# Performance work log

Hardware: AMD Instinct MI355X
Metric: run time of the kernel (lower is better)

Reference implementation:

```python
import jax, jax.numpy as jnp
import numpy as np

N_HEADS = 16

def setup_inputs() -> dict:
    key = jax.random.key(0)
    qkv = jax.random.normal(key, (4, 3072, 1024), dtype=jnp.float32)
    return {"qkv": qkv}

def reference(qkv):
    bs, width, length = qkv.shape
    ch = width // (3 * N_HEADS)
    qkv_h = qkv.reshape(bs * N_HEADS, 3 * ch, length)
    q, k, v = jnp.split(qkv_h, 3, axis=1)  # each [bs*H, ch, T]
    scale = 1.0 / jnp.sqrt(jnp.sqrt(jnp.asarray(ch, qkv.dtype)))
    # [bs*H, T, T] scores
    weight = jnp.einsum('bct,bcs->bts', q * scale, k * scale)
    weight = jax.nn.softmax(weight.astype(jnp.float32), axis=-1).astype(weight.dtype)
    a = jnp.einsum('bts,bcs->bct', weight, v)  # [bs*H, ch, T]
    return a.reshape(bs, -1, length)
```

## Files before the change

### kernel.cpp

```cpp
#include <hip/hip_runtime.h>
#include <hip/hip_bf16.h>


typedef __bf16 bf16_8 __attribute__((ext_vector_type(8)));
typedef __bf16 bf16_4 __attribute__((ext_vector_type(4)));
typedef float floatx4 __attribute__((ext_vector_type(4)));

#define NTHREADS 256
#define STRIDE 72
#define NSTEPS 16

#if __has_builtin(__builtin_amdgcn_exp2f)
#define EXP2(x) __builtin_amdgcn_exp2f(x)
#else
#define EXP2(x) exp2f(x)
#endif
#define QSCALE 0.18033688011112042f

#define LDS_BYTES 36864

__global__ __launch_bounds__(NTHREADS, 2)
void attn_kernel(const float* __restrict__ qkv, float* __restrict__ out) {
    __shared__ char smem[LDS_BYTES];
    __bf16* q_s = (__bf16*)smem;
    __bf16* k_s = (__bf16*)(smem + 18432);
    __bf16* v_s = (__bf16*)(smem + 27648);

    const int tid  = threadIdx.x;
    const int wave = tid >> 6;
    const int lane = tid & 63;
    const int quad = lane >> 4;
    const int i16  = lane & 15;

    const int bx = blockIdx.x;
    const int bh = bx & 63;
    const int t0 = (bx >> 6) << 7;

    const float* qg = qkv + (size_t)bh * 196608;
    const float* kg = qg + 65536;
    const float* vg = qg + 131072;

    int sc[4], ss4[4], goff[4], swz[4];
    #pragma unroll
    for (int j = 0; j < 4; ++j) {
        int f   = j * NTHREADS + tid;
        sc[j]   = f >> 4;
        ss4[j]  = (f & 15) << 2;
        goff[j] = sc[j] * 1024 + ss4[j];
        swz[j]  = sc[j] ^ ((f & 7) << 3);
    }

    #pragma unroll
    for (int j = 0; j < 8; ++j) {
        int f  = j * NTHREADS + tid;
        int c  = f >> 5;
        int t4 = (f & 31) << 2;
        int sq = c ^ ((f & 7) << 3);
        float4 q4 = *(const float4*)(qg + c * 1024 + t0 + t4);
        q_s[(t4 + 0) * STRIDE + sq] = (__bf16)(q4.x * QSCALE);
        q_s[(t4 + 1) * STRIDE + sq] = (__bf16)(q4.y * QSCALE);
        q_s[(t4 + 2) * STRIDE + sq] = (__bf16)(q4.z * QSCALE);
        q_s[(t4 + 3) * STRIDE + sq] = (__bf16)(q4.w * QSCALE);
    }
    #pragma unroll
    for (int j = 0; j < 4; ++j) {
        float4 k4 = *(const float4*)(kg + goff[j]);
        k_s[(ss4[j] + 0) * STRIDE + swz[j]] = (__bf16)k4.x;
        k_s[(ss4[j] + 1) * STRIDE + swz[j]] = (__bf16)k4.y;
        k_s[(ss4[j] + 2) * STRIDE + swz[j]] = (__bf16)k4.z;
        k_s[(ss4[j] + 3) * STRIDE + swz[j]] = (__bf16)k4.w;
        float4 v4 = *(const float4*)(vg + goff[j]);
        bf16_4 pv;
        pv[0] = (__bf16)v4.x; pv[1] = (__bf16)v4.y;
        pv[2] = (__bf16)v4.z; pv[3] = (__bf16)v4.w;
        *(bf16_4*)&v_s[sc[j] * STRIDE + ss4[j]] = pv;
    }
    __syncthreads();

    bf16_8 qf[2][2];
    #pragma unroll
    for (int tt = 0; tt < 2; ++tt) {
        int row = wave * 32 + tt * 16 + i16;
        int x = (row >> 2) & 7;
        #pragma unroll
        for (int kk = 0; kk < 2; ++kk)
            qf[tt][kk] = *(const bf16_8*)&q_s[row * STRIDE + ((((kk << 2) | quad) ^ x) << 3)];
    }

    floatx4 O[2][4];
    #pragma unroll
    for (int tt = 0; tt < 2; ++tt)
        #pragma unroll
        for (int cn = 0; cn < 4; ++cn) O[tt][cn] = (floatx4){0.f, 0.f, 0.f, 0.f};
    float l[2] = {0.f, 0.f};

    __bf16* pw = q_s + (size_t)(wave * 32) * STRIDE;

    for (int is = 0; is < NSTEPS; ++is) {
        float4 kr[4], vr[4];
        if (is < NSTEPS - 1) {
            const int s0n = (is + 1) * 64;
            #pragma unroll
            for (int j = 0; j < 4; ++j) {
                kr[j] = *(const float4*)(kg + goff[j] + s0n);
                vr[j] = *(const float4*)(vg + goff[j] + s0n);
            }
        }

        floatx4 St[2][4];
        #pragma unroll
        for (int sb = 0; sb < 4; ++sb) {
            floatx4 a0 = (floatx4){0.f, 0.f, 0.f, 0.f};
            floatx4 a1 = (floatx4){0.f, 0.f, 0.f, 0.f};
            int row = sb * 16 + i16;
            int x = (row >> 2) & 7;
            #pragma unroll
            for (int kk = 0; kk < 2; ++kk) {
                bf16_8 kf = *(const bf16_8*)&k_s[row * STRIDE + ((((kk << 2) | quad) ^ x) << 3)];
                a0 = __builtin_amdgcn_mfma_f32_16x16x32_bf16(kf, qf[0][kk], a0, 0, 0, 0);
                a1 = __builtin_amdgcn_mfma_f32_16x16x32_bf16(kf, qf[1][kk], a1, 0, 0, 0);
            }
            St[0][sb] = a0;
            St[1][sb] = a1;
        }
        #pragma unroll
        for (int tt = 0; tt < 2; ++tt)
            #pragma unroll
            for (int sb = 0; sb < 4; ++sb) {
                float p0 = EXP2(St[tt][sb][0]);
                float p1 = EXP2(St[tt][sb][1]);
                float p2 = EXP2(St[tt][sb][2]);
                float p3 = EXP2(St[tt][sb][3]);
                l[tt] += (p0 + p1) + (p2 + p3);
                bf16_4 pk;
                pk[0] = (__bf16)p0; pk[1] = (__bf16)p1;
                pk[2] = (__bf16)p2; pk[3] = (__bf16)p3;
                *(bf16_4*)&pw[(tt * 16 + i16) * STRIDE + sb * 16 + quad * 4] = pk;
            }
        bf16_8 af[2][2];
        #pragma unroll
        for (int tt = 0; tt < 2; ++tt)
            #pragma unroll
            for (int kk = 0; kk < 2; ++kk)
                af[tt][kk] = *(const bf16_8*)&pw[(tt * 16 + i16) * STRIDE + kk * 32 + quad * 8];
        #pragma unroll
        for (int cn = 0; cn < 4; ++cn)
            #pragma unroll
            for (int kk = 0; kk < 2; ++kk) {
                bf16_8 vf = *(const bf16_8*)&v_s[(cn * 16 + i16) * STRIDE + kk * 32 + quad * 8];
                O[0][cn] = __builtin_amdgcn_mfma_f32_16x16x32_bf16(vf, af[0][kk], O[0][cn], 0, 0, 0);
                O[1][cn] = __builtin_amdgcn_mfma_f32_16x16x32_bf16(vf, af[1][kk], O[1][cn], 0, 0, 0);
            }

        if (is < NSTEPS - 1) {
            __syncthreads();
            #pragma unroll
            for (int j = 0; j < 4; ++j) {
                k_s[(ss4[j] + 0) * STRIDE + swz[j]] = (__bf16)kr[j].x;
                k_s[(ss4[j] + 1) * STRIDE + swz[j]] = (__bf16)kr[j].y;
                k_s[(ss4[j] + 2) * STRIDE + swz[j]] = (__bf16)kr[j].z;
                k_s[(ss4[j] + 3) * STRIDE + swz[j]] = (__bf16)kr[j].w;
                bf16_4 pv;
                pv[0] = (__bf16)vr[j].x; pv[1] = (__bf16)vr[j].y;
                pv[2] = (__bf16)vr[j].z; pv[3] = (__bf16)vr[j].w;
                *(bf16_4*)&v_s[sc[j] * STRIDE + ss4[j]] = pv;
            }
            __syncthreads();
        }
    }

    float* og = out + (size_t)bh * 65536 + t0 + wave * 32;
    #pragma unroll
    for (int tt = 0; tt < 2; ++tt) {
        float s = l[tt];
        s += __shfl_xor(s, 16);
        s += __shfl_xor(s, 32);
        const float linv = 1.0f / s;
        #pragma unroll
        for (int cn = 0; cn < 4; ++cn)
            #pragma unroll
            for (int r = 0; r < 4; ++r)
                og[(cn * 16 + 4 * quad + r) * 1024 + tt * 16 + i16] = O[tt][cn][r] * linv;
    }
}

extern "C" void kernel_launch(void* const* d_in, const int* in_sizes, int n_in,
                              void* d_out, int out_size, void* d_ws, size_t ws_size,
                              hipStream_t stream) {
    const float* qkv = (const float*)d_in[0];
    float* out = (float*)d_out;
    attn_kernel<<<dim3(512), dim3(NTHREADS), 0, stream>>>(qkv, out);
}
```

Measured before the change: 109.7 us.

## Double query tile per block and transpose K staging into 4-wide LDS stores

Each block now handles 256 query rows instead of 128, with each wave owning 64 rows, so every K/V tile staged in LDS feeds twice as many MFMAs and global K/V traffic halves. The grid shrinks from 512 to 256 blocks. K and Q are now written to LDS with packed 4-element bf16 stores using a new XOR swizzle instead of scalar transposed stores. The cost is more accumulator registers and fewer blocks on a 256-CU device, which leaves at most one block per CU and reduces latency hiding.

```diff
diff --git a/kernel.cpp b/kernel.cpp
--- a/kernel.cpp
+++ b/kernel.cpp
@@ -17,14 +17,14 @@
 #endif
 #define QSCALE 0.18033688011112042f
 
-#define LDS_BYTES 36864
+#define LDS_BYTES 55296
 
 __global__ __launch_bounds__(NTHREADS, 2)
 void attn_kernel(const float* __restrict__ qkv, float* __restrict__ out) {
     __shared__ char smem[LDS_BYTES];
     __bf16* q_s = (__bf16*)smem;
-    __bf16* k_s = (__bf16*)(smem + 18432);
-    __bf16* v_s = (__bf16*)(smem + 27648);
+    __bf16* k_s = (__bf16*)(smem + 36864);
+    __bf16* v_s = (__bf16*)(smem + 46080);
 
     const int tid  = threadIdx.x;
     const int wave = tid >> 6;
@@ -34,97 +34,107 @@
 
     const int bx = blockIdx.x;
     const int bh = bx & 63;
-    const int t0 = (bx >> 6) << 7;
+    const int t0 = (bx >> 6) << 8;
 
     const float* qg = qkv + (size_t)bh * 196608;
     const float* kg = qg + 65536;
     const float* vg = qg + 131072;
 
-    int sc[4], ss4[4], goff[4], swz[4];
-    #pragma unroll
-    for (int j = 0; j < 4; ++j) {
-        int f   = j * NTHREADS + tid;
-        sc[j]   = f >> 4;
-        ss4[j]  = (f & 15) << 2;
-        goff[j] = sc[j] * 1024 + ss4[j];
-        swz[j]  = sc[j] ^ ((f & 7) << 3);
-    }
-
-    #pragma unroll
-    for (int j = 0; j < 8; ++j) {
-        int f  = j * NTHREADS + tid;
-        int c  = f >> 5;
-        int t4 = (f & 31) << 2;
-        int sq = c ^ ((f & 7) << 3);
-        float4 q4 = *(const float4*)(qg + c * 1024 + t0 + t4);
-        q_s[(t4 + 0) * STRIDE + sq] = (__bf16)(q4.x * QSCALE);
-        q_s[(t4 + 1) * STRIDE + sq] = (__bf16)(q4.y * QSCALE);
-        q_s[(t4 + 2) * STRIDE + sq] = (__bf16)(q4.z * QSCALE);
-        q_s[(t4 + 3) * STRIDE + sq] = (__bf16)(q4.w * QSCALE);
-    }
-    #pragma unroll
-    for (int j = 0; j < 4; ++j) {
-        float4 k4 = *(const float4*)(kg + goff[j]);
-        k_s[(ss4[j] + 0) * STRIDE + swz[j]] = (__bf16)k4.x;
-        k_s[(ss4[j] + 1) * STRIDE + swz[j]] = (__bf16)k4.y;
-        k_s[(ss4[j] + 2) * STRIDE + swz[j]] = (__bf16)k4.z;
-        k_s[(ss4[j] + 3) * STRIDE + swz[j]] = (__bf16)k4.w;
-        float4 v4 = *(const float4*)(vg + goff[j]);
-        bf16_4 pv;
-        pv[0] = (__bf16)v4.x; pv[1] = (__bf16)v4.y;
-        pv[2] = (__bf16)v4.z; pv[3] = (__bf16)v4.w;
-        *(bf16_4*)&v_s[sc[j] * STRIDE + ss4[j]] = pv;
+    const int si = tid & 15;
+    const int sG = tid >> 4;
+    const int c0 = sG << 2;
+
+    #pragma unroll
+    for (int tj = 0; tj < 4; ++tj) {
+        float4 q4[4];
+        #pragma unroll
+        for (int jj = 0; jj < 4; ++jj)
+            q4[jj] = *(const float4*)(qg + (c0 + jj) * 1024 + t0 + tj * 64 + si * 4);
+        #pragma unroll
+        for (int rr = 0; rr < 4; ++rr) {
+            int trow = tj * 64 + si * 4 + rr;
+            bf16_4 w;
+            w[0] = (__bf16)(((const float*)&q4[0])[rr] * QSCALE);
+            w[1] = (__bf16)(((const float*)&q4[1])[rr] * QSCALE);
+            w[2] = (__bf16)(((const float*)&q4[2])[rr] * QSCALE);
+            w[3] = (__bf16)(((const float*)&q4[3])[rr] * QSCALE);
+            *(bf16_4*)&q_s[trow * STRIDE + ((sG ^ (trow & 14)) << 2)] = w;
+        }
+    }
+    {
+        float4 k4[4], v4[4];
+        #pragma unroll
+        for (int jj = 0; jj < 4; ++jj) {
+            k4[jj] = *(const float4*)(kg + (c0 + jj) * 1024 + si * 4);
+            v4[jj] = *(const float4*)(vg + (c0 + jj) * 1024 + si * 4);
+        }
+        #pragma unroll
+        for (int rr = 0; rr < 4; ++rr) {
+            int srow = si * 4 + rr;
+            bf16_4 w;
+            w[0] = (__bf16)((const float*)&k4[0])[rr];
+            w[1] = (__bf16)((const float*)&k4[1])[rr];
+            w[2] = (__bf16)((const float*)&k4[2])[rr];
+            w[3] = (__bf16)((const float*)&k4[3])[rr];
+            *(bf16_4*)&k_s[srow * STRIDE + ((sG ^ (srow & 14)) << 2)] = w;
+        }
+        #pragma unroll
+        for (int jj = 0; jj < 4; ++jj) {
+            bf16_4 w;
+            w[0] = (__bf16)v4[jj].x; w[1] = (__bf16)v4[jj].y;
+            w[2] = (__bf16)v4[jj].z; w[3] = (__bf16)v4[jj].w;
+            *(bf16_4*)&v_s[(c0 + jj) * STRIDE + si * 4] = w;
+        }
     }
     __syncthreads();
 
-    bf16_8 qf[2][2];
-    #pragma unroll
-    for (int tt = 0; tt < 2; ++tt) {
-        int row = wave * 32 + tt * 16 + i16;
-        int x = (row >> 2) & 7;
+    bf16_8 qf[4][2];
+    #pragma unroll
+    for (int tt = 0; tt < 4; ++tt) {
+        int row = wave * 64 + tt * 16 + i16;
+        int e2 = (row >> 1) & 7;
         #pragma unroll
         for (int kk = 0; kk < 2; ++kk)
-            qf[tt][kk] = *(const bf16_8*)&q_s[row * STRIDE + ((((kk << 2) | quad) ^ x) << 3)];
-    }
-
-    floatx4 O[2][4];
-    #pragma unroll
-    for (int tt = 0; tt < 2; ++tt)
+            qf[tt][kk] = *(const bf16_8*)&q_s[row * STRIDE + (((kk * 4 + quad) ^ e2) << 3)];
+    }
+
+    floatx4 O[4][4];
+    #pragma unroll
+    for (int tt = 0; tt < 4; ++tt)
         #pragma unroll
         for (int cn = 0; cn < 4; ++cn) O[tt][cn] = (floatx4){0.f, 0.f, 0.f, 0.f};
-    float l[2] = {0.f, 0.f};
-
-    __bf16* pw = q_s + (size_t)(wave * 32) * STRIDE;
+    float l[4] = {0.f, 0.f, 0.f, 0.f};
+
+    __bf16* pw = q_s + (size_t)(wave * 64) * STRIDE;
 
     for (int is = 0; is < NSTEPS; ++is) {
         float4 kr[4], vr[4];
         if (is < NSTEPS - 1) {
             const int s0n = (is + 1) * 64;
             #pragma unroll
-            for (int j = 0; j < 4; ++j) {
-                kr[j] = *(const float4*)(kg + goff[j] + s0n);
-                vr[j] = *(const float4*)(vg + goff[j] + s0n);
-            }
-        }
-
-        floatx4 St[2][4];
+            for (int jj = 0; jj < 4; ++jj) {
+                kr[jj] = *(const float4*)(kg + (c0 + jj) * 1024 + s0n + si * 4);
+                vr[jj] = *(const float4*)(vg + (c0 + jj) * 1024 + s0n + si * 4);
+            }
+        }
+
+        floatx4 St[4][4];
         #pragma unroll
         for (int sb = 0; sb < 4; ++sb) {
-            floatx4 a0 = (floatx4){0.f, 0.f, 0.f, 0.f};
-            floatx4 a1 = (floatx4){0.f, 0.f, 0.f, 0.f};
-            int row = sb * 16 + i16;
-            int x = (row >> 2) & 7;
-            #pragma unroll
-            for (int kk = 0; kk < 2; ++kk) {
-                bf16_8 kf = *(const bf16_8*)&k_s[row * STRIDE + ((((kk << 2) | quad) ^ x) << 3)];
-                a0 = __builtin_amdgcn_mfma_f32_16x16x32_bf16(kf, qf[0][kk], a0, 0, 0, 0);
-                a1 = __builtin_amdgcn_mfma_f32_16x16x32_bf16(kf, qf[1][kk], a1, 0, 0, 0);
-            }
-            St[0][sb] = a0;
-            St[1][sb] = a1;
-        }
-        #pragma unroll
-        for (int tt = 0; tt < 2; ++tt)
+            int srow = sb * 16 + i16;
+            int e2 = (srow >> 1) & 7;
+            bf16_8 kf0 = *(const bf16_8*)&k_s[srow * STRIDE + ((quad ^ e2) << 3)];
+            bf16_8 kf1 = *(const bf16_8*)&k_s[srow * STRIDE + (((4 + quad) ^ e2) << 3)];
+            #pragma unroll
+            for (int tt = 0; tt < 4; ++tt) {
+                floatx4 acc = __builtin_amdgcn_mfma_f32_16x16x32_bf16(
+                    kf0, qf[tt][0], (floatx4){0.f, 0.f, 0.f, 0.f}, 0, 0, 0);
+                St[tt][sb] = __builtin_amdgcn_mfma_f32_16x16x32_bf16(
+                    kf1, qf[tt][1], acc, 0, 0, 0);
+            }
+        }
+        #pragma unroll
+        for (int tt = 0; tt < 4; ++tt)
             #pragma unroll
             for (int sb = 0; sb < 4; ++sb) {
                 float p0 = EXP2(St[tt][sb][0]);
@@ -137,9 +147,9 @@
                 pk[2] = (__bf16)p2; pk[3] = (__bf16)p3;
                 *(bf16_4*)&pw[(tt * 16 + i16) * STRIDE + sb * 16 + quad * 4] = pk;
             }
-        bf16_8 af[2][2];
-        #pragma unroll
-        for (int tt = 0; tt < 2; ++tt)
+        bf16_8 af[4][2];
+        #pragma unroll
+        for (int tt = 0; tt < 4; ++tt)
             #pragma unroll
             for (int kk = 0; kk < 2; ++kk)
                 af[tt][kk] = *(const bf16_8*)&pw[(tt * 16 + i16) * STRIDE + kk * 32 + quad * 8];
@@ -148,30 +158,38 @@
             #pragma unroll
             for (int kk = 0; kk < 2; ++kk) {
                 bf16_8 vf = *(const bf16_8*)&v_s[(cn * 16 + i16) * STRIDE + kk * 32 + quad * 8];
-                O[0][cn] = __builtin_amdgcn_mfma_f32_16x16x32_bf16(vf, af[0][kk], O[0][cn], 0, 0, 0);
-                O[1][cn] = __builtin_amdgcn_mfma_f32_16x16x32_bf16(vf, af[1][kk], O[1][cn], 0, 0, 0);
+                #pragma unroll
+                for (int tt = 0; tt < 4; ++tt)
+                    O[tt][cn] = __builtin_amdgcn_mfma_f32_16x16x32_bf16(
+                        vf, af[tt][kk], O[tt][cn], 0, 0, 0);
             }
 
         if (is < NSTEPS - 1) {
             __syncthreads();
             #pragma unroll
-            for (int j = 0; j < 4; ++j) {
-                k_s[(ss4[j] + 0) * STRIDE + swz[j]] = (__bf16)kr[j].x;
-                k_s[(ss4[j] + 1) * STRIDE + swz[j]] = (__bf16)kr[j].y;
-                k_s[(ss4[j] + 2) * STRIDE + swz[j]] = (__bf16)kr[j].z;
-                k_s[(ss4[j] + 3) * STRIDE + swz[j]] = (__bf16)kr[j].w;
-                bf16_4 pv;
-                pv[0] = (__bf16)vr[j].x; pv[1] = (__bf16)vr[j].y;
-                pv[2] = (__bf16)vr[j].z; pv[3] = (__bf16)vr[j].w;
-                *(bf16_4*)&v_s[sc[j] * STRIDE + ss4[j]] = pv;
+            for (int rr = 0; rr < 4; ++rr) {
+                int srow = si * 4 + rr;
+                bf16_4 w;
+                w[0] = (__bf16)((const float*)&kr[0])[rr];
+                w[1] = (__bf16)((const float*)&kr[1])[rr];
+                w[2] = (__bf16)((const float*)&kr[2])[rr];
+                w[3] = (__bf16)((const float*)&kr[3])[rr];
+                *(bf16_4*)&k_s[srow * STRIDE + ((sG ^ (srow & 14)) << 2)] = w;
+            }
+            #pragma unroll
+            for (int jj = 0; jj < 4; ++jj) {
+                bf16_4 w;
+                w[0] = (__bf16)vr[jj].x; w[1] = (__bf16)vr[jj].y;
+                w[2] = (__bf16)vr[jj].z; w[3] = (__bf16)vr[jj].w;
+                *(bf16_4*)&v_s[(c0 + jj) * STRIDE + si * 4] = w;
             }
             __syncthreads();
         }
     }
 
-    float* og = out + (size_t)bh * 65536 + t0 + wave * 32;
-    #pragma unroll
-    for (int tt = 0; tt < 2; ++tt) {
+    float* og = out + (size_t)bh * 65536 + t0 + wave * 64;
+    #pragma unroll
+    for (int tt = 0; tt < 4; ++tt) {
         float s = l[tt];
         s += __shfl_xor(s, 16);
         s += __shfl_xor(s, 32);
@@ -189,5 +207,5 @@
                               hipStream_t stream) {
     const float* qkv = (const float*)d_in[0];
     float* out = (float*)d_out;
-    attn_kernel<<<dim3(512), dim3(NTHREADS), 0, stream>>>(qkv, out);
+    attn_kernel<<<dim3(256), dim3(NTHREADS), 0, stream>>>(qkv, out);
 }
```

After: 114.9 us. 1.05x slower.
